# Performance work log

Hardware: AMD Instinct MI355X
Metric: run time of the kernel (lower is better)

The kernel has to match this reference:

```python
import jax, jax.numpy as jnp
import numpy as np

B, C, H, W = 2, 64, 256, 256
CQ = C // 8    # query/key channels
CR = C // 16   # ShareChannelAttention reduction


def _conv1x1(x, w, b):
    # x: [B,C,H,W], w: [O,C], b: [O]  (1x1 conv == per-pixel linear)
    return jnp.einsum('bchw,oc->bohw', x, w) + b[None, :, None, None]


def _criss_cross(q, k, v):
    # q,k: [B,CQ,H,W], v: [B,C,H,W]; row+column attention with -inf on the
    # H-diagonal, softmax over concatenated H+W energies.
    Hh = q.shape[2]
    eH = jnp.einsum('bchw,bcgw->bhwg', q, k)                 # column (over h') energies
    eH = jnp.where(jnp.eye(Hh, dtype=bool)[:, None, :], -jnp.inf, eH)
    eW = jnp.einsum('bchw,bchv->bhwv', q, k)                 # row (over w') energies
    att = jax.nn.softmax(jnp.concatenate([eH, eW], axis=-1), axis=-1)  # [B,H,W,H+W]
    aH, aW = att[..., :Hh], att[..., Hh:]
    outH = jnp.einsum('bhwg,bcgw->bchw', aH, v)
    outW = jnp.einsum('bhwv,bchv->bchw', aW, v)
    return outH + outW


def _shareca(xa, xb, w1, b1, w2, b2):
    s = xa + xb
    def mlp(p):
        return _conv1x1(jax.nn.relu(_conv1x1(p, w1, b1)), w2, b2)
    gate = jax.nn.sigmoid(mlp(s.mean(axis=(2, 3), keepdims=True)) +
                          mlp(s.max(axis=(2, 3), keepdims=True)))
    return gate * s  # gate*xa + gate*xb


def _bn_relu(x, scale, bias):
    # BatchNorm2d in training mode (batch statistics, biased variance), eps=1e-5
    m = x.mean(axis=(0, 2, 3), keepdims=True)
    v = x.var(axis=(0, 2, 3), keepdims=True)
    xn = (x - m) * jax.lax.rsqrt(v + 1e-5)
    return jax.nn.relu(xn * scale[None, :, None, None] + bias[None, :, None, None])


def setup_inputs() -> dict:
    key = jax.random.key(0)
    ks = jax.random.split(key, 32)
    def n(k, shape, s=0.05):
        return jax.random.normal(k, shape, dtype=jnp.float32) * s
    inp = {
        'x1': n(ks[0], (B, C, H, W), 1.0),
        'x2': n(ks[1], (B, C, H, W), 1.0),
        'wq1': n(ks[2], (CQ, C)), 'bq1': n(ks[3], (CQ,)),
        'wq2': n(ks[4], (CQ, C)), 'bq2': n(ks[5], (CQ,)),
        'wk1': n(ks[6], (CQ, C)), 'bk1': n(ks[7], (CQ,)),
        'wk2': n(ks[8], (CQ, C)), 'bk2': n(ks[9], (CQ,)),
        'wv1': n(ks[10], (C, C)), 'bv1': n(ks[11], (C,)),
        'wv2': n(ks[12], (C, C)), 'bv2': n(ks[13], (C,)),
        'gamma1': n(ks[14], (1,), 0.5), 'gamma2': n(ks[15], (1,), 0.5),
        'sc1_w1': n(ks[16], (CR, C)), 'sc1_b1': n(ks[17], (CR,)),
        'sc1_w2': n(ks[18], (C, CR)), 'sc1_b2': n(ks[19], (C,)),
        'sc2_w1': n(ks[20], (CR, C)), 'sc2_b1': n(ks[21], (CR,)),
        'sc2_w2': n(ks[22], (C, CR)), 'sc2_b2': n(ks[23], (C,)),
        'bn1_scale': jnp.ones((C,), jnp.float32), 'bn1_bias': n(ks[24], (C,)),
        'bn2_scale': jnp.ones((C,), jnp.float32), 'bn2_bias': n(ks[25], (C,)),
    }
    return inp


def reference(x1, x2, wq1, bq1, wq2, bq2, wk1, bk1, wk2, bk2,
              wv1, bv1, wv2, bv2, gamma1, gamma2,
              sc1_w1, sc1_b1, sc1_w2, sc1_b2,
              sc2_w1, sc2_b1, sc2_w2, sc2_b2,
              bn1_scale, bn1_bias, bn2_scale, bn2_bias):
    q1 = _conv1x1(x1, wq1, bq1); q2 = _conv1x1(x2, wq2, bq2)
    k1 = _conv1x1(x1, wk1, bk1); k2 = _conv1x1(x2, wk2, bk2)
    v1 = _conv1x1(x1, wv1, bv1); v2 = _conv1x1(x2, wv2, bv2)
    att1 = _criss_cross(q2, k1, v1)  # out_H_1 + out_W_1
    att2 = _criss_cross(q1, k2, v2)  # out_H_2 + out_W_2
    x_1 = _shareca(gamma2 * att2 + x2, x1, sc1_w1, sc1_b1, sc1_w2, sc1_b2)
    x_2 = _shareca(gamma1 * att1 + x1, x2, sc2_w1, sc2_b1, sc2_w2, sc2_b2)
    out1 = _bn_relu(x_1 + x1, bn1_scale, bn1_bias)
    out2 = _bn_relu(x_2 + x2, bn2_scale, bn2_bias)
    # channel exchange: even channels keep the original input
    mask = (jnp.arange(C) % 2 == 0)[None, :, None, None]
    return jnp.where(mask, x1, out1), jnp.where(mask, x2, out2)
```

## Files before the change

kernel.cpp:

```cpp
#include <hip/hip_runtime.h>
#include <hip/hip_bf16.h>
#include <cstdint>
#include <cstddef>

typedef unsigned short bf16t;
typedef __attribute__((ext_vector_type(8))) short bf16x8;
typedef __attribute__((ext_vector_type(4))) float f32x4;

__device__ __forceinline__ unsigned short f2bf(float f) {
    unsigned u = __float_as_uint(f);
    u += 0x7fffu + ((u >> 16) & 1u);
    return (unsigned short)(u >> 16);
}
__device__ __forceinline__ float bf2f(unsigned short h) {
    return __uint_as_float(((unsigned)h) << 16);
}
__device__ __forceinline__ float bflo(unsigned u) { return __uint_as_float(u << 16); }
__device__ __forceinline__ float bfhi(unsigned u) { return __uint_as_float(u & 0xffff0000u); }
__device__ __forceinline__ unsigned pk2(float a, float b) {
    __hip_bfloat162 h = __float22bfloat162_rn(make_float2(a, b));
    return *(unsigned*)&h;
}
__device__ __forceinline__ bf16x8 mk8(unsigned a, unsigned b, unsigned c, unsigned d) {
    union { uint4 u; bf16x8 v; } cv; cv.u = make_uint4(a, b, c, d); return cv.v;
}

__device__ __forceinline__ unsigned fenc(float f) {
    unsigned u = __float_as_uint(f);
    return (u & 0x80000000u) ? ~u : (u | 0x80000000u);
}
__device__ __forceinline__ float fdec(unsigned u) {
    return __uint_as_float((u & 0x80000000u) ? (u ^ 0x80000000u) : ~u);
}

#define HW 65536

struct ConvArgs {
    const float* x[2];
    const float* wq[2]; const float* bq[2];
    const float* wk[2]; const float* bk[2];
    const float* wv[2]; const float* bv[2];
    bf16t* q[2]; bf16t* k[2]; bf16t* v[2];
    unsigned* zeroR;
};

__global__ __launch_bounds__(256) void conv_qkv(ConvArgs A)
{
    __shared__ __align__(16) bf16t Xlds[256 * 68];

    const int t = threadIdx.x;
    const int z = blockIdx.z;
    const int s = z >> 1, b = z & 1;
    if (z == 0 && blockIdx.x == 0) {
#pragma unroll
        for (int i = 0; i < 6; i++) A.zeroR[t + i * 256] = 0u;
    }
    const int lane = t & 63, wv = t >> 6, quad = lane >> 4, l16 = lane & 15;
    const int px0 = blockIdx.x * 256;

    const float* xp = A.x[s] + (size_t)b * 64 * HW + px0 + t;
    {
        unsigned xw[32];
#pragma unroll
        for (int c = 0; c < 32; c++)
            xw[c] = pk2(xp[(size_t)(2 * c) * HW], xp[(size_t)(2 * c + 1) * HW]);
#pragma unroll
        for (int g = 0; g < 16; g++)
            *(uint2*)&Xlds[t * 68 + g * 4] = make_uint2(xw[2 * g], xw[2 * g + 1]);
    }

    bf16x8 bfr[5][2];
    float bo[5];
    bf16t* obase[5];
#pragma unroll
    for (int ot = 0; ot < 5; ot++) {
        const int o = ot * 16 + l16;
        const float* wrow;
        if (o < 8)       { wrow = A.wq[s] + o * 64;        bo[ot] = A.bq[s][o];
                           obase[ot] = A.q[s] + (size_t)(b * 8 + o) * HW; }
        else if (o < 16) { wrow = A.wk[s] + (o - 8) * 64;  bo[ot] = A.bk[s][o - 8];
                           obase[ot] = A.k[s] + (size_t)(b * 8 + o - 8) * HW; }
        else             { wrow = A.wv[s] + (o - 16) * 64; bo[ot] = A.bv[s][o - 16];
                           obase[ot] = A.v[s] + (size_t)(b * 64 + o - 16) * HW; }
#pragma unroll
        for (int ks = 0; ks < 2; ks++) {
            const float* wp = wrow + ks * 32 + quad * 8;
            bfr[ot][ks] = mk8(pk2(wp[0], wp[1]), pk2(wp[2], wp[3]),
                              pk2(wp[4], wp[5]), pk2(wp[6], wp[7]));
        }
    }

    __syncthreads();

    bf16x8 afr[4][2];
#pragma unroll
    for (int i = 0; i < 4; i++)
#pragma unroll
        for (int ks = 0; ks < 2; ks++) {
            const int base = (wv * 64 + i * 16 + l16) * 68 + ks * 32 + quad * 8;
            const uint2 lo = *(const uint2*)&Xlds[base];
            const uint2 hi = *(const uint2*)&Xlds[base + 4];
            afr[i][ks] = mk8(lo.x, lo.y, hi.x, hi.y);
        }

    const f32x4 z4 = {0.f, 0.f, 0.f, 0.f};
    f32x4 acc[4][5];
#pragma unroll
    for (int i = 0; i < 4; i++)
#pragma unroll
        for (int ot = 0; ot < 5; ot++) acc[i][ot] = z4;

#pragma unroll
    for (int ks = 0; ks < 2; ks++)
#pragma unroll
        for (int i = 0; i < 4; i++)
#pragma unroll
            for (int ot = 0; ot < 5; ot++)
                acc[i][ot] = __builtin_amdgcn_mfma_f32_16x16x32_bf16(afr[i][ks], bfr[ot][ks], acc[i][ot], 0, 0, 0);

#pragma unroll
    for (int i = 0; i < 4; i++) {
        const int px = px0 + wv * 64 + i * 16 + quad * 4;
#pragma unroll
        for (int ot = 0; ot < 5; ot++) {
            uint2 u;
            u.x = pk2(acc[i][ot][0] + bo[ot], acc[i][ot][1] + bo[ot]);
            u.y = pk2(acc[i][ot][2] + bo[ot], acc[i][ot][3] + bo[ot]);
            *(uint2*)&obase[ot][px] = u;
        }
    }
}

__global__ __launch_bounds__(256) void transpose16(const bf16t* __restrict__ in, bf16t* __restrict__ out)
{
    __shared__ bf16t tile[64][68];
    const size_t zo = (size_t)blockIdx.z * HW;
    const int i0 = blockIdx.y * 64, j0 = blockIdx.x * 64;
    const int lc = threadIdx.x & 63, rg = threadIdx.x >> 6;
#pragma unroll
    for (int rr = 0; rr < 16; rr++) {
        int row = rg * 16 + rr;
        tile[row][lc] = in[zo + (size_t)(i0 + row) * 256 + j0 + lc];
    }
    __syncthreads();
#pragma unroll
    for (int rr = 0; rr < 16; rr++) {
        int row = rg * 16 + rr;
        out[zo + (size_t)(j0 + row) * 256 + i0 + lc] = tile[lc][row];
    }
}

struct RowccArgs {
    const bf16t* q[4]; const bf16t* k[4]; const bf16t* v[4];
    bf16t* o[4]; float* so[4];
};

__global__ __launch_bounds__(256, 3) void rowcc_mfma(RowccArgs P)
{
    __shared__ __align__(16) char smem[54272];
    bf16t* vs = (bf16t*)smem;
    bf16t* ps = (bf16t*)(smem + 33792);

    const int t = threadIdx.x;
    const int r = blockIdx.x, b = blockIdx.y, z = blockIdx.z;
    const bool mask = (z < 2);
    const int lane = t & 63, wv = t >> 6, quad = lane >> 4, l16 = lane & 15;
    const int wband = wv * 64;

    const bf16t* qp = P.q[z];
    const bf16t* kp = P.k[z];
    const bf16t* vp = P.v[z];

    const size_t vb = (size_t)b * 64 * HW + (size_t)r * 256;
#pragma unroll
    for (int i = 0; i < 8; i++) {
        const int qd = i * 256 + t;
        const int c = qd >> 5, jc = (qd & 31) * 8;
        *(uint4*)&vs[c * 264 + jc] = *(const uint4*)&vp[vb + (size_t)c * HW + jc];
    }

    const bf16x8 zfr = {0, 0, 0, 0, 0, 0, 0, 0};
    bf16x8 qfr[4] = {zfr, zfr, zfr, zfr};
    const size_t rowb = (size_t)b * 8 * HW + (size_t)r * 256;
    if (quad == 0) {
#pragma unroll
        for (int wt = 0; wt < 4; wt++) {
            const int w_g = wband + wt * 16 + l16;
#pragma unroll
            for (int ch = 0; ch < 8; ch++)
                qfr[wt][ch] = (short)qp[rowb + (size_t)ch * HW + w_g];
        }
    }

    const f32x4 z4 = {0.f, 0.f, 0.f, 0.f};
    f32x4 acc[4][4];
#pragma unroll
    for (int i = 0; i < 4; i++)
#pragma unroll
        for (int j = 0; j < 4; j++) acc[i][j] = z4;
    float s_t[4] = {0.f, 0.f, 0.f, 0.f};

    bf16x8 kcur[2] = {zfr, zfr};
    if (quad == 0) {
#pragma unroll
        for (int jtile = 0; jtile < 2; jtile++)
#pragma unroll
            for (int ch = 0; ch < 8; ch++)
                kcur[jtile][ch] = (short)kp[rowb + (size_t)ch * HW + jtile * 16 + l16];
    }

    __syncthreads();

    for (int jt = 0; jt < 8; jt++) {
        const int j0 = jt * 32;
        f32x4 e[4][2];
#pragma unroll
        for (int wt = 0; wt < 4; wt++)
#pragma unroll
            for (int jtile = 0; jtile < 2; jtile++)
                e[wt][jtile] = __builtin_amdgcn_mfma_f32_16x16x32_bf16(kcur[jtile], qfr[wt], z4, 0, 0, 0);

        bf16x8 knext[2] = {zfr, zfr};
        if (jt < 7 && quad == 0) {
            const int jn = (jt + 1) * 32;
#pragma unroll
            for (int jtile = 0; jtile < 2; jtile++)
#pragma unroll
                for (int ch = 0; ch < 8; ch++)
                    knext[jtile][ch] = (short)kp[rowb + (size_t)ch * HW + jn + jtile * 16 + l16];
        }

        if (mask && (jt >> 1) == wv) {
#pragma unroll
            for (int wt = 0; wt < 4; wt++) {
                const int w_g = wband + wt * 16 + l16;
#pragma unroll
                for (int jtile = 0; jtile < 2; jtile++)
#pragma unroll
                    for (int rr = 0; rr < 4; rr++)
                        if (j0 + jtile * 16 + quad * 4 + rr == w_g) e[wt][jtile][rr] = -3.0e38f;
            }
        }

#pragma unroll
        for (int wt = 0; wt < 4; wt++) {
#pragma unroll
            for (int jtile = 0; jtile < 2; jtile++) {
                const float p0 = __expf(e[wt][jtile][0]);
                const float p1 = __expf(e[wt][jtile][1]);
                const float p2 = __expf(e[wt][jtile][2]);
                const float p3 = __expf(e[wt][jtile][3]);
                s_t[wt] += (p0 + p1) + (p2 + p3);
                uint2 u; u.x = pk2(p0, p1); u.y = pk2(p2, p3);
                *(uint2*)&ps[(wband + wt * 16 + l16) * 40 + jtile * 16 + quad * 4] = u;
            }
        }

        bf16x8 afr[4], bfr[4];
#pragma unroll
        for (int wt = 0; wt < 4; wt++)
            afr[wt] = *(const bf16x8*)&ps[(wband + wt * 16 + l16) * 40 + quad * 8];
#pragma unroll
        for (int ct = 0; ct < 4; ct++)
            bfr[ct] = *(const bf16x8*)&vs[(ct * 16 + l16) * 264 + j0 + quad * 8];
#pragma unroll
        for (int wt = 0; wt < 4; wt++)
#pragma unroll
            for (int ct = 0; ct < 4; ct++)
                acc[wt][ct] = __builtin_amdgcn_mfma_f32_16x16x32_bf16(afr[wt], bfr[ct], acc[wt][ct], 0, 0, 0);

        kcur[0] = knext[0]; kcur[1] = knext[1];
    }

#pragma unroll
    for (int wt = 0; wt < 4; wt++) {
        float s = s_t[wt];
        s += __shfl_xor(s, 16, 64);
        s += __shfl_xor(s, 32, 64);
        s_t[wt] = s;
    }
    if (quad == 0) {
#pragma unroll
        for (int wt = 0; wt < 4; wt++) {
            const int w_g = wband + wt * 16 + l16;
            if (mask)
                P.so[z][(size_t)b * HW + w_g * 256 + r] = s_t[wt];
            else
                P.so[z][(size_t)b * HW + r * 256 + w_g] = s_t[wt];
        }
    }

    __syncthreads();
    bf16t* o_lds = (bf16t*)smem;
#pragma unroll
    for (int wt = 0; wt < 4; wt++) {
        const int w0 = wband + wt * 16 + quad * 4;
#pragma unroll
        for (int ct = 0; ct < 4; ct++) {
            const int c = ct * 16 + l16;
            uint2 u;
            u.x = pk2(acc[wt][ct][0], acc[wt][ct][1]);
            u.y = pk2(acc[wt][ct][2], acc[wt][ct][3]);
            *(uint2*)&o_lds[c * 264 + w0] = u;
        }
    }
    __syncthreads();
    bf16t* ob = P.o[z] + (size_t)b * 64 * HW + (size_t)r * 256;
#pragma unroll
    for (int i = 0; i < 8; i++) {
        const int qd = i * 256 + t;
        const int c = qd >> 5, w8 = (qd & 31) * 8;
        *(uint4*)&ob[(size_t)c * HW + w8] = *(const uint4*)&o_lds[c * 264 + w8];
    }
}

__global__ __launch_bounds__(256) void combine_reduce(
    const bf16t* __restrict__ oH1, const bf16t* __restrict__ oW1,
    const bf16t* __restrict__ oH2, const bf16t* __restrict__ oW2,
    const float* __restrict__ sH1, const float* __restrict__ sW1,
    const float* __restrict__ sH2, const float* __restrict__ sW2,
    const float* __restrict__ x1, const float* __restrict__ x2,
    const float* __restrict__ gamma1, const float* __restrict__ gamma2,
    bf16t* __restrict__ s1, bf16t* __restrict__ s2,
    float* __restrict__ accum, unsigned* __restrict__ accmax)
{
    const int t = threadIdx.x, chunk = blockIdx.x, c = blockIdx.y, b = blockIdx.z;
    const float g1v = gamma1[0], g2v = gamma2[0];
    const size_t cb = ((size_t)(b * 64 + c)) * HW;
    const size_t pb = (size_t)b * HW;

    float pS1 = 0, pSS1 = 0, pSX1 = 0, pX1 = 0, pXX1 = 0, pM1 = -3e38f;
    float pS2 = 0, pSS2 = 0, pSX2 = 0, pX2 = 0, pXX2 = 0, pM2 = -3e38f;

    for (int i = 0; i < 16; i++) {
        const int pidx = chunk * 4096 + i * 256 + t;
        const float inv1 = 1.f / (sH1[pb + pidx] + sW1[pb + pidx]);
        const float inv2 = 1.f / (sH2[pb + pidx] + sW2[pb + pidx]);
        const float a1 = (bf2f(oH1[cb + pidx]) + bf2f(oW1[cb + pidx])) * inv1;
        const float a2 = (bf2f(oH2[cb + pidx]) + bf2f(oW2[cb + pidx])) * inv2;
        const float x1v = x1[cb + pidx], x2v = x2[cb + pidx];
        const float s1v = g2v * a2 + x2v + x1v;
        const float s2v = g1v * a1 + x1v + x2v;
        s1[cb + pidx] = f2bf(s1v);
        s2[cb + pidx] = f2bf(s2v);
        pS1 += s1v; pSS1 += s1v * s1v; pSX1 += s1v * x1v; pX1 += x1v; pXX1 += x1v * x1v; pM1 = fmaxf(pM1, s1v);
        pS2 += s2v; pSS2 += s2v * s2v; pSX2 += s2v * x2v; pX2 += x2v; pXX2 += x2v * x2v; pM2 = fmaxf(pM2, s2v);
    }

    __shared__ float wred[12][4];
    float vals[12] = {pS1, pSS1, pSX1, pX1, pXX1, pM1, pS2, pSS2, pSX2, pX2, pXX2, pM2};
    const int lane = t & 63, wave = t >> 6;
#pragma unroll
    for (int iv = 0; iv < 12; iv++) {
        float v = vals[iv];
        const bool isMax = (iv == 5 || iv == 11);
#pragma unroll
        for (int off = 32; off > 0; off >>= 1) {
            const float o = __shfl_down(v, off, 64);
            v = isMax ? fmaxf(v, o) : (v + o);
        }
        if (lane == 0) wred[iv][wave] = v;
    }
    __syncthreads();
    if (t < 12) {
        const bool isMax = (t == 5 || t == 11);
        float v = wred[t][0];
        for (int i = 1; i < 4; i++) v = isMax ? fmaxf(v, wred[t][i]) : (v + wred[t][i]);
        const int stream = (t >= 6) ? 1 : 0;
        const int kk = t - stream * 6;
        if (kk == 5) atomicMax(&accmax[(stream * 2 + b) * 64 + c], fenc(v));
        else atomicAdd(&accum[((stream * 2 + b) * 64 + c) * 5 + kk], v);
    }
}

__global__ __launch_bounds__(256) void gates_bn(
    const float* __restrict__ accum, const unsigned* __restrict__ accmax,
    const float* __restrict__ sc1_w1, const float* __restrict__ sc1_b1,
    const float* __restrict__ sc1_w2, const float* __restrict__ sc1_b2,
    const float* __restrict__ sc2_w1, const float* __restrict__ sc2_b1,
    const float* __restrict__ sc2_w2, const float* __restrict__ sc2_b2,
    const float* __restrict__ bn1_scale, const float* __restrict__ bn1_bias,
    const float* __restrict__ bn2_scale, const float* __restrict__ bn2_bias,
    float* __restrict__ gates, float* __restrict__ AB)
{
    const int t = threadIdx.x;
    const int stream = t >> 7, b = (t >> 6) & 1, c = t & 63;
    __shared__ float meanS[256], maxS[256], e1S[256], e2S[256];

    const float S = accum[t * 5 + 0], SS = accum[t * 5 + 1], SX = accum[t * 5 + 2];
    const float X = accum[t * 5 + 3], XX = accum[t * 5 + 4];
    meanS[t] = S * (1.f / 65536.f);
    maxS[t] = fdec(accmax[t]);
    __syncthreads();

    const float* w1 = stream ? sc2_w1 : sc1_w1;
    const float* b1 = stream ? sc2_b1 : sc1_b1;
    const float* w2 = stream ? sc2_w2 : sc1_w2;
    const float* b2 = stream ? sc2_b2 : sc1_b2;
    float om = b2[c], ox = b2[c];
    const int base = stream * 128 + b * 64;
#pragma unroll
    for (int r = 0; r < 4; r++) {
        float hm = b1[r], hx = b1[r];
        for (int cc = 0; cc < 64; cc++) {
            hm += w1[r * 64 + cc] * meanS[base + cc];
            hx += w1[r * 64 + cc] * maxS[base + cc];
        }
        hm = fmaxf(hm, 0.f); hx = fmaxf(hx, 0.f);
        om += w2[c * 4 + r] * hm;
        ox += w2[c * 4 + r] * hx;
    }
    const float gate = 1.f / (1.f + __expf(-(om + ox)));
    gates[t] = gate;
    e1S[t] = gate * S + X;
    e2S[t] = gate * gate * SS + 2.f * gate * SX + XX;
    __syncthreads();
    if (b == 0) {
        const float sumY = e1S[t] + e1S[t + 64];
        const float sumY2 = e2S[t] + e2S[t + 64];
        const float meanY = sumY * (1.f / 131072.f);
        const float varY = sumY2 * (1.f / 131072.f) - meanY * meanY;
        const float sc = stream ? bn2_scale[c] : bn1_scale[c];
        const float bi = stream ? bn2_bias[c] : bn1_bias[c];
        const float A = sc * rsqrtf(varY + 1e-5f);
        AB[stream * 128 + c] = A;
        AB[stream * 128 + 64 + c] = bi - meanY * A;
    }
}

__global__ __launch_bounds__(256) void finalize(
    const bf16t* __restrict__ s1, const bf16t* __restrict__ s2,
    const float* __restrict__ x1, const float* __restrict__ x2,
    const float* __restrict__ gates, const float* __restrict__ AB,
    float* __restrict__ out)
{
    const size_t tid = (size_t)blockIdx.x * 256 + threadIdx.x;
    const size_t idx = tid * 4;
    const int b = (int)(idx >> 22);
    const int c = (int)((idx >> 16) & 63);
    const bool odd = (c & 1) != 0;
    const float g1 = gates[b * 64 + c], g2 = gates[128 + b * 64 + c];
    const float A1 = AB[c], B1 = AB[64 + c], A2 = AB[128 + c], B2 = AB[192 + c];

    const uint2 su1 = *(const uint2*)(s1 + idx);
    const uint2 su2 = *(const uint2*)(s2 + idx);
    const float4 x1v = *(const float4*)(x1 + idx);
    const float4 x2v = *(const float4*)(x2 + idx);
    float s1f[4] = {bflo(su1.x), bfhi(su1.x), bflo(su1.y), bfhi(su1.y)};
    float s2f[4] = {bflo(su2.x), bfhi(su2.x), bflo(su2.y), bfhi(su2.y)};
    float xa[4] = {x1v.x, x1v.y, x1v.z, x1v.w};
    float xb[4] = {x2v.x, x2v.y, x2v.z, x2v.w};
    float o1[4], o2[4];
#pragma unroll
    for (int j = 0; j < 4; j++) {
        const float y1 = g1 * s1f[j] + xa[j];
        const float y2 = g2 * s2f[j] + xb[j];
        o1[j] = odd ? fmaxf(A1 * y1 + B1, 0.f) : xa[j];
        o2[j] = odd ? fmaxf(A2 * y2 + B2, 0.f) : xb[j];
    }
    *(float4*)(out + idx) = make_float4(o1[0], o1[1], o1[2], o1[3]);
    *(float4*)(out + 8388608 + idx) = make_float4(o2[0], o2[1], o2[2], o2[3]);
}

extern "C" void kernel_launch(void* const* d_in, const int* in_sizes, int n_in,
                              void* d_out, int out_size, void* d_ws, size_t ws_size,
                              hipStream_t stream) {
    (void)in_sizes; (void)n_in; (void)out_size; (void)ws_size;
    const float* x1 = (const float*)d_in[0];
    const float* x2 = (const float*)d_in[1];
    const float* wq1 = (const float*)d_in[2];  const float* bq1 = (const float*)d_in[3];
    const float* wq2 = (const float*)d_in[4];  const float* bq2 = (const float*)d_in[5];
    const float* wk1 = (const float*)d_in[6];  const float* bk1 = (const float*)d_in[7];
    const float* wk2 = (const float*)d_in[8];  const float* bk2 = (const float*)d_in[9];
    const float* wv1 = (const float*)d_in[10]; const float* bv1 = (const float*)d_in[11];
    const float* wv2 = (const float*)d_in[12]; const float* bv2 = (const float*)d_in[13];
    const float* gamma1 = (const float*)d_in[14];
    const float* gamma2 = (const float*)d_in[15];
    const float* sc1_w1 = (const float*)d_in[16]; const float* sc1_b1 = (const float*)d_in[17];
    const float* sc1_w2 = (const float*)d_in[18]; const float* sc1_b2 = (const float*)d_in[19];
    const float* sc2_w1 = (const float*)d_in[20]; const float* sc2_b1 = (const float*)d_in[21];
    const float* sc2_w2 = (const float*)d_in[22]; const float* sc2_b2 = (const float*)d_in[23];
    const float* bn1_scale = (const float*)d_in[24]; const float* bn1_bias = (const float*)d_in[25];
    const float* bn2_scale = (const float*)d_in[26]; const float* bn2_bias = (const float*)d_in[27];

    char* p = (char*)d_ws;
    const size_t SZ_QK = 2097152;
    const size_t SZ_V = 16777216;
    const size_t SZ_ST = 524288;

    bf16t* q1 = (bf16t*)(p + 0 * SZ_QK);
    bf16t* k1 = (bf16t*)(p + 1 * SZ_QK);
    bf16t* q2 = (bf16t*)(p + 2 * SZ_QK);
    bf16t* k2 = (bf16t*)(p + 3 * SZ_QK);
    bf16t* v1 = (bf16t*)(p + 4 * SZ_QK);
    bf16t* v2 = (bf16t*)(p + 4 * SZ_QK + SZ_V);
    size_t off = 4 * SZ_QK + 2 * SZ_V;
    bf16t* q1T = (bf16t*)(p + off + 0 * SZ_QK);
    bf16t* k1T = (bf16t*)(p + off + 1 * SZ_QK);
    bf16t* q2T = (bf16t*)(p + off + 2 * SZ_QK);
    bf16t* k2T = (bf16t*)(p + off + 3 * SZ_QK);
    bf16t* v1T = (bf16t*)(p + off + 4 * SZ_QK);
    bf16t* v2T = (bf16t*)(p + off + 4 * SZ_QK + SZ_V);
    off += 4 * SZ_QK + 2 * SZ_V;
    bf16t* oH1T = (bf16t*)(p + off); off += SZ_V;
    bf16t* oH2T = (bf16t*)(p + off); off += SZ_V;
    bf16t* oW1 = (bf16t*)(p + off); off += SZ_V;
    bf16t* oW2 = (bf16t*)(p + off); off += SZ_V;
    float* sH1 = (float*)(p + off); off += SZ_ST;
    float* sH2 = (float*)(p + off); off += SZ_ST;
    float* sW1 = (float*)(p + off); off += SZ_ST;
    float* sW2 = (float*)(p + off); off += SZ_ST;
    float* accum = (float*)(p + off);
    unsigned* accmax = (unsigned*)(p + off + 5120);
    float* gates = (float*)(p + off + 6144);
    float* AB = (float*)(p + off + 7168);

    bf16t* oH1 = v1T;
    bf16t* oH2 = v2T;
    bf16t* s1 = oH1T;
    bf16t* s2 = oH2T;

    ConvArgs CA;
    CA.x[0] = x1; CA.x[1] = x2;
    CA.wq[0] = wq1; CA.wq[1] = wq2; CA.bq[0] = bq1; CA.bq[1] = bq2;
    CA.wk[0] = wk1; CA.wk[1] = wk2; CA.bk[0] = bk1; CA.bk[1] = bk2;
    CA.wv[0] = wv1; CA.wv[1] = wv2; CA.bv[0] = bv1; CA.bv[1] = bv2;
    CA.q[0] = q1; CA.q[1] = q2; CA.k[0] = k1; CA.k[1] = k2;
    CA.v[0] = v1; CA.v[1] = v2;
    CA.zeroR = (unsigned*)accum;
    conv_qkv<<<dim3(256, 1, 4), 256, 0, stream>>>(CA);

    transpose16<<<dim3(4, 4, 320), 256, 0, stream>>>(q1, q1T);

    RowccArgs RA;
    RA.q[0] = q2T; RA.k[0] = k1T; RA.v[0] = v1T; RA.o[0] = oH1T; RA.so[0] = sH1;
    RA.q[1] = q1T; RA.k[1] = k2T; RA.v[1] = v2T; RA.o[1] = oH2T; RA.so[1] = sH2;
    RA.q[2] = q2;  RA.k[2] = k1;  RA.v[2] = v1;  RA.o[2] = oW1;  RA.so[2] = sW1;
    RA.q[3] = q1;  RA.k[3] = k2;  RA.v[3] = v2;  RA.o[3] = oW2;  RA.so[3] = sW2;
    rowcc_mfma<<<dim3(256, 2, 4), 256, 0, stream>>>(RA);

    transpose16<<<dim3(4, 4, 256), 256, 0, stream>>>(oH1T, oH1);

    combine_reduce<<<dim3(16, 64, 2), 256, 0, stream>>>(
        oH1, oW1, oH2, oW2, sH1, sW1, sH2, sW2, x1, x2, gamma1, gamma2,
        s1, s2, accum, accmax);

    gates_bn<<<1, 256, 0, stream>>>(accum, accmax,
                                    sc1_w1, sc1_b1, sc1_w2, sc1_b2,
                                    sc2_w1, sc2_b1, sc2_w2, sc2_b2,
                                    bn1_scale, bn1_bias, bn2_scale, bn2_bias,
                                    gates, AB);

    finalize<<<8192, 256, 0, stream>>>(s1, s2, x1, x2, gates, AB, (float*)d_out);
}
```

Before: 323.4 us.

## Fold log2e into Q, stage K/Q in LDS, pipeline scores, fuse gates and drop transpose

The attention kernel now stages the K and Q rows in LDS and computes the next tile's scores while the PV MFMAs run, using exp2 with log2e folded into the query conv weights. The transpose of the column-attention output is removed; combine_reduce reads the transposed layout directly. The separate gates/BN kernel is merged into combine_reduce through a last-block-done atomic counter. The changes cut launches, extra memory passes and exp cost, but combine_reduce now reads with a strided access pattern and rowcc occupancy drops from 3 to 2 blocks.

```diff
diff --git a/kernel.cpp b/kernel.cpp
--- a/kernel.cpp
+++ b/kernel.cpp
@@ -24,7 +24,6 @@
 __device__ __forceinline__ bf16x8 mk8(unsigned a, unsigned b, unsigned c, unsigned d) {
     union { uint4 u; bf16x8 v; } cv; cv.u = make_uint4(a, b, c, d); return cv.v;
 }
-
 __device__ __forceinline__ unsigned fenc(float f) {
     unsigned u = __float_as_uint(f);
     return (u & 0x80000000u) ? ~u : (u | 0x80000000u);
@@ -34,6 +33,7 @@
 }
 
 #define HW 65536
+#define LOG2E 1.4426950408889634f
 
 struct ConvArgs {
     const float* x[2];
@@ -53,7 +53,7 @@
     const int s = z >> 1, b = z & 1;
     if (z == 0 && blockIdx.x == 0) {
 #pragma unroll
-        for (int i = 0; i < 6; i++) A.zeroR[t + i * 256] = 0u;
+        for (int i = 0; i < 7; i++) A.zeroR[t + i * 256] = 0u;
     }
     const int lane = t & 63, wv = t >> 6, quad = lane >> 4, l16 = lane & 15;
     const int px0 = blockIdx.x * 256;
@@ -76,7 +76,8 @@
     for (int ot = 0; ot < 5; ot++) {
         const int o = ot * 16 + l16;
         const float* wrow;
-        if (o < 8)       { wrow = A.wq[s] + o * 64;        bo[ot] = A.bq[s][o];
+        float wsc = 1.f;
+        if (o < 8)       { wrow = A.wq[s] + o * 64;        bo[ot] = A.bq[s][o] * LOG2E; wsc = LOG2E;
                            obase[ot] = A.q[s] + (size_t)(b * 8 + o) * HW; }
         else if (o < 16) { wrow = A.wk[s] + (o - 8) * 64;  bo[ot] = A.bk[s][o - 8];
                            obase[ot] = A.k[s] + (size_t)(b * 8 + o - 8) * HW; }
@@ -85,8 +86,8 @@
 #pragma unroll
         for (int ks = 0; ks < 2; ks++) {
             const float* wp = wrow + ks * 32 + quad * 8;
-            bfr[ot][ks] = mk8(pk2(wp[0], wp[1]), pk2(wp[2], wp[3]),
-                              pk2(wp[4], wp[5]), pk2(wp[6], wp[7]));
+            bfr[ot][ks] = mk8(pk2(wp[0] * wsc, wp[1] * wsc), pk2(wp[2] * wsc, wp[3] * wsc),
+                              pk2(wp[4] * wsc, wp[5] * wsc), pk2(wp[6] * wsc, wp[7] * wsc));
         }
     }
 
@@ -155,11 +156,13 @@
     bf16t* o[4]; float* so[4];
 };
 
-__global__ __launch_bounds__(256, 3) void rowcc_mfma(RowccArgs P)
+__global__ __launch_bounds__(256, 2) void rowcc_mfma(RowccArgs P)
 {
-    __shared__ __align__(16) char smem[54272];
+    __shared__ __align__(16) char smem[62464];
     bf16t* vs = (bf16t*)smem;
     bf16t* ps = (bf16t*)(smem + 33792);
+    bf16t* ks = (bf16t*)(smem + 54272);
+    bf16t* qs = (bf16t*)(smem + 58368);
 
     const int t = threadIdx.x;
     const int r = blockIdx.x, b = blockIdx.y, z = blockIdx.z;
@@ -171,6 +174,21 @@
     const bf16t* kp = P.k[z];
     const bf16t* vp = P.v[z];
 
+    const size_t rowb = (size_t)b * 8 * HW + (size_t)r * 256 + t;
+    {
+        const bf16t* kq = kp + rowb;
+        unsigned w0 = (unsigned)kq[0] | ((unsigned)kq[(size_t)HW] << 16);
+        unsigned w1 = (unsigned)kq[2 * (size_t)HW] | ((unsigned)kq[3 * (size_t)HW] << 16);
+        unsigned w2 = (unsigned)kq[4 * (size_t)HW] | ((unsigned)kq[5 * (size_t)HW] << 16);
+        unsigned w3 = (unsigned)kq[6 * (size_t)HW] | ((unsigned)kq[7 * (size_t)HW] << 16);
+        *(uint4*)&ks[t * 8] = make_uint4(w0, w1, w2, w3);
+        const bf16t* qq = qp + rowb;
+        w0 = (unsigned)qq[0] | ((unsigned)qq[(size_t)HW] << 16);
+        w1 = (unsigned)qq[2 * (size_t)HW] | ((unsigned)qq[3 * (size_t)HW] << 16);
+        w2 = (unsigned)qq[4 * (size_t)HW] | ((unsigned)qq[5 * (size_t)HW] << 16);
+        w3 = (unsigned)qq[6 * (size_t)HW] | ((unsigned)qq[7 * (size_t)HW] << 16);
+        *(uint4*)&qs[t * 8] = make_uint4(w0, w1, w2, w3);
+    }
     const size_t vb = (size_t)b * 64 * HW + (size_t)r * 256;
 #pragma unroll
     for (int i = 0; i < 8; i++) {
@@ -179,20 +197,17 @@
         *(uint4*)&vs[c * 264 + jc] = *(const uint4*)&vp[vb + (size_t)c * HW + jc];
     }
 
+    __syncthreads();
+
     const bf16x8 zfr = {0, 0, 0, 0, 0, 0, 0, 0};
-    bf16x8 qfr[4] = {zfr, zfr, zfr, zfr};
-    const size_t rowb = (size_t)b * 8 * HW + (size_t)r * 256;
-    if (quad == 0) {
-#pragma unroll
-        for (int wt = 0; wt < 4; wt++) {
-            const int w_g = wband + wt * 16 + l16;
-#pragma unroll
-            for (int ch = 0; ch < 8; ch++)
-                qfr[wt][ch] = (short)qp[rowb + (size_t)ch * HW + w_g];
-        }
-    }
-
     const f32x4 z4 = {0.f, 0.f, 0.f, 0.f};
+    bf16x8 qfr[4];
+#pragma unroll
+    for (int wt = 0; wt < 4; wt++) {
+        bf16x8 v8 = *(const bf16x8*)&qs[(wband + wt * 16 + l16) * 8];
+        qfr[wt] = (quad == 0) ? v8 : zfr;
+    }
+
     f32x4 acc[4][4];
 #pragma unroll
     for (int i = 0; i < 4; i++)
@@ -200,37 +215,18 @@
         for (int j = 0; j < 4; j++) acc[i][j] = z4;
     float s_t[4] = {0.f, 0.f, 0.f, 0.f};
 
-    bf16x8 kcur[2] = {zfr, zfr};
-    if (quad == 0) {
-#pragma unroll
-        for (int jtile = 0; jtile < 2; jtile++)
-#pragma unroll
-            for (int ch = 0; ch < 8; ch++)
-                kcur[jtile][ch] = (short)kp[rowb + (size_t)ch * HW + jtile * 16 + l16];
-    }
-
-    __syncthreads();
-
-    for (int jt = 0; jt < 8; jt++) {
-        const int j0 = jt * 32;
-        f32x4 e[4][2];
-#pragma unroll
-        for (int wt = 0; wt < 4; wt++)
-#pragma unroll
-            for (int jtile = 0; jtile < 2; jtile++)
-                e[wt][jtile] = __builtin_amdgcn_mfma_f32_16x16x32_bf16(kcur[jtile], qfr[wt], z4, 0, 0, 0);
-
-        bf16x8 knext[2] = {zfr, zfr};
-        if (jt < 7 && quad == 0) {
-            const int jn = (jt + 1) * 32;
-#pragma unroll
-            for (int jtile = 0; jtile < 2; jtile++)
-#pragma unroll
-                for (int ch = 0; ch < 8; ch++)
-                    knext[jtile][ch] = (short)kp[rowb + (size_t)ch * HW + jn + jtile * 16 + l16];
-        }
-
+    auto scores = [&](int jt, f32x4 (&e)[4][2]) {
+        bf16x8 kfr0 = *(const bf16x8*)&ks[(jt * 32 + l16) * 8];
+        bf16x8 kfr1 = *(const bf16x8*)&ks[(jt * 32 + 16 + l16) * 8];
+#pragma unroll
+        for (int wt = 0; wt < 4; wt++) {
+            e[wt][0] = __builtin_amdgcn_mfma_f32_16x16x32_bf16(kfr0, qfr[wt], z4, 0, 0, 0);
+            e[wt][1] = __builtin_amdgcn_mfma_f32_16x16x32_bf16(kfr1, qfr[wt], z4, 0, 0, 0);
+        }
+    };
+    auto expstore = [&](int jt, f32x4 (&e)[4][2]) {
         if (mask && (jt >> 1) == wv) {
+            const int j0m = jt * 32;
 #pragma unroll
             for (int wt = 0; wt < 4; wt++) {
                 const int w_g = wband + wt * 16 + l16;
@@ -238,24 +234,32 @@
                 for (int jtile = 0; jtile < 2; jtile++)
 #pragma unroll
                     for (int rr = 0; rr < 4; rr++)
-                        if (j0 + jtile * 16 + quad * 4 + rr == w_g) e[wt][jtile][rr] = -3.0e38f;
+                        if (j0m + jtile * 16 + quad * 4 + rr == w_g) e[wt][jtile][rr] = -3.0e38f;
             }
         }
-
 #pragma unroll
         for (int wt = 0; wt < 4; wt++) {
 #pragma unroll
             for (int jtile = 0; jtile < 2; jtile++) {
-                const float p0 = __expf(e[wt][jtile][0]);
-                const float p1 = __expf(e[wt][jtile][1]);
-                const float p2 = __expf(e[wt][jtile][2]);
-                const float p3 = __expf(e[wt][jtile][3]);
+                const float p0 = __builtin_amdgcn_exp2f(e[wt][jtile][0]);
+                const float p1 = __builtin_amdgcn_exp2f(e[wt][jtile][1]);
+                const float p2 = __builtin_amdgcn_exp2f(e[wt][jtile][2]);
+                const float p3 = __builtin_amdgcn_exp2f(e[wt][jtile][3]);
                 s_t[wt] += (p0 + p1) + (p2 + p3);
                 uint2 u; u.x = pk2(p0, p1); u.y = pk2(p2, p3);
                 *(uint2*)&ps[(wband + wt * 16 + l16) * 40 + jtile * 16 + quad * 4] = u;
             }
         }
-
+    };
+
+    {
+        f32x4 e0[4][2];
+        scores(0, e0);
+        expstore(0, e0);
+    }
+
+    for (int jt = 0; jt < 8; jt++) {
+        const int j0 = jt * 32;
         bf16x8 afr[4], bfr[4];
 #pragma unroll
         for (int wt = 0; wt < 4; wt++)
@@ -263,13 +267,17 @@
 #pragma unroll
         for (int ct = 0; ct < 4; ct++)
             bfr[ct] = *(const bf16x8*)&vs[(ct * 16 + l16) * 264 + j0 + quad * 8];
+
+        f32x4 en[4][2];
+        if (jt < 7) scores(jt + 1, en);
+
 #pragma unroll
         for (int wt = 0; wt < 4; wt++)
 #pragma unroll
             for (int ct = 0; ct < 4; ct++)
                 acc[wt][ct] = __builtin_amdgcn_mfma_f32_16x16x32_bf16(afr[wt], bfr[ct], acc[wt][ct], 0, 0, 0);
 
-        kcur[0] = knext[0]; kcur[1] = knext[1];
+        if (jt < 7) expstore(jt + 1, en);
     }
 
 #pragma unroll
@@ -283,10 +291,7 @@
 #pragma unroll
         for (int wt = 0; wt < 4; wt++) {
             const int w_g = wband + wt * 16 + l16;
-            if (mask)
-                P.so[z][(size_t)b * HW + w_g * 256 + r] = s_t[wt];
-            else
-                P.so[z][(size_t)b * HW + r * 256 + w_g] = s_t[wt];
+            P.so[z][(size_t)b * HW + r * 256 + w_g] = s_t[wt];
         }
     }
 
@@ -315,14 +320,21 @@
 }
 
 __global__ __launch_bounds__(256) void combine_reduce(
-    const bf16t* __restrict__ oH1, const bf16t* __restrict__ oW1,
-    const bf16t* __restrict__ oH2, const bf16t* __restrict__ oW2,
-    const float* __restrict__ sH1, const float* __restrict__ sW1,
-    const float* __restrict__ sH2, const float* __restrict__ sW2,
+    const bf16t* __restrict__ oH1T, const bf16t* __restrict__ oW1,
+    const bf16t* __restrict__ oH2T, const bf16t* __restrict__ oW2,
+    const float* __restrict__ sH1T, const float* __restrict__ sW1,
+    const float* __restrict__ sH2T, const float* __restrict__ sW2,
     const float* __restrict__ x1, const float* __restrict__ x2,
     const float* __restrict__ gamma1, const float* __restrict__ gamma2,
     bf16t* __restrict__ s1, bf16t* __restrict__ s2,
-    float* __restrict__ accum, unsigned* __restrict__ accmax)
+    float* __restrict__ accum, unsigned* __restrict__ accmax, unsigned* __restrict__ done,
+    const float* __restrict__ sc1_w1, const float* __restrict__ sc1_b1,
+    const float* __restrict__ sc1_w2, const float* __restrict__ sc1_b2,
+    const float* __restrict__ sc2_w1, const float* __restrict__ sc2_b1,
+    const float* __restrict__ sc2_w2, const float* __restrict__ sc2_b2,
+    const float* __restrict__ bn1_scale, const float* __restrict__ bn1_bias,
+    const float* __restrict__ bn2_scale, const float* __restrict__ bn2_bias,
+    float* __restrict__ gates, float* __restrict__ AB)
 {
     const int t = threadIdx.x, chunk = blockIdx.x, c = blockIdx.y, b = blockIdx.z;
     const float g1v = gamma1[0], g2v = gamma2[0];
@@ -333,11 +345,14 @@
     float pS2 = 0, pSS2 = 0, pSX2 = 0, pX2 = 0, pXX2 = 0, pM2 = -3e38f;
 
     for (int i = 0; i < 16; i++) {
-        const int pidx = chunk * 4096 + i * 256 + t;
-        const float inv1 = 1.f / (sH1[pb + pidx] + sW1[pb + pidx]);
-        const float inv2 = 1.f / (sH2[pb + pidx] + sW2[pb + pidx]);
-        const float a1 = (bf2f(oH1[cb + pidx]) + bf2f(oW1[cb + pidx])) * inv1;
-        const float a2 = (bf2f(oH2[cb + pidx]) + bf2f(oW2[cb + pidx])) * inv2;
+        const int h = chunk * 16 + i;
+        const int pidx = h * 256 + t;
+        const size_t tI = pb + (size_t)t * 256 + h;
+        const size_t trI = cb + (size_t)t * 256 + h;
+        const float inv1 = 1.f / (sH1T[tI] + sW1[pb + pidx]);
+        const float inv2 = 1.f / (sH2T[tI] + sW2[pb + pidx]);
+        const float a1 = (bf2f(oH1T[trI]) + bf2f(oW1[cb + pidx])) * inv1;
+        const float a2 = (bf2f(oH2T[trI]) + bf2f(oW2[cb + pidx])) * inv2;
         const float x1v = x1[cb + pidx], x2v = x2[cb + pidx];
         const float s1v = g2v * a2 + x2v + x1v;
         const float s2v = g1v * a1 + x1v + x2v;
@@ -371,60 +386,60 @@
         if (kk == 5) atomicMax(&accmax[(stream * 2 + b) * 64 + c], fenc(v));
         else atomicAdd(&accum[((stream * 2 + b) * 64 + c) * 5 + kk], v);
     }
-}
-
-__global__ __launch_bounds__(256) void gates_bn(
-    const float* __restrict__ accum, const unsigned* __restrict__ accmax,
-    const float* __restrict__ sc1_w1, const float* __restrict__ sc1_b1,
-    const float* __restrict__ sc1_w2, const float* __restrict__ sc1_b2,
-    const float* __restrict__ sc2_w1, const float* __restrict__ sc2_b1,
-    const float* __restrict__ sc2_w2, const float* __restrict__ sc2_b2,
-    const float* __restrict__ bn1_scale, const float* __restrict__ bn1_bias,
-    const float* __restrict__ bn2_scale, const float* __restrict__ bn2_bias,
-    float* __restrict__ gates, float* __restrict__ AB)
-{
-    const int t = threadIdx.x;
-    const int stream = t >> 7, b = (t >> 6) & 1, c = t & 63;
+
+    __threadfence();
+    __shared__ int lastFlag;
+    __syncthreads();
+    if (t == 0) lastFlag = (atomicAdd(done, 1u) == 2047u) ? 1 : 0;
+    __syncthreads();
+    if (!lastFlag) return;
+    __threadfence();
+
     __shared__ float meanS[256], maxS[256], e1S[256], e2S[256];
-
-    const float S = accum[t * 5 + 0], SS = accum[t * 5 + 1], SX = accum[t * 5 + 2];
-    const float X = accum[t * 5 + 3], XX = accum[t * 5 + 4];
-    meanS[t] = S * (1.f / 65536.f);
-    maxS[t] = fdec(accmax[t]);
-    __syncthreads();
-
-    const float* w1 = stream ? sc2_w1 : sc1_w1;
-    const float* b1 = stream ? sc2_b1 : sc1_b1;
-    const float* w2 = stream ? sc2_w2 : sc1_w2;
-    const float* b2 = stream ? sc2_b2 : sc1_b2;
-    float om = b2[c], ox = b2[c];
-    const int base = stream * 128 + b * 64;
-#pragma unroll
-    for (int r = 0; r < 4; r++) {
-        float hm = b1[r], hx = b1[r];
-        for (int cc = 0; cc < 64; cc++) {
-            hm += w1[r * 64 + cc] * meanS[base + cc];
-            hx += w1[r * 64 + cc] * maxS[base + cc];
-        }
-        hm = fmaxf(hm, 0.f); hx = fmaxf(hx, 0.f);
-        om += w2[c * 4 + r] * hm;
-        ox += w2[c * 4 + r] * hx;
-    }
-    const float gate = 1.f / (1.f + __expf(-(om + ox)));
-    gates[t] = gate;
-    e1S[t] = gate * S + X;
-    e2S[t] = gate * gate * SS + 2.f * gate * SX + XX;
-    __syncthreads();
-    if (b == 0) {
-        const float sumY = e1S[t] + e1S[t + 64];
-        const float sumY2 = e2S[t] + e2S[t + 64];
-        const float meanY = sumY * (1.f / 131072.f);
-        const float varY = sumY2 * (1.f / 131072.f) - meanY * meanY;
-        const float sc = stream ? bn2_scale[c] : bn1_scale[c];
-        const float bi = stream ? bn2_bias[c] : bn1_bias[c];
-        const float A = sc * rsqrtf(varY + 1e-5f);
-        AB[stream * 128 + c] = A;
-        AB[stream * 128 + 64 + c] = bi - meanY * A;
+    {
+        const int stream = t >> 7, bb = (t >> 6) & 1, cc = t & 63;
+        const float S  = atomicAdd(&accum[t * 5 + 0], 0.f);
+        const float SS = atomicAdd(&accum[t * 5 + 1], 0.f);
+        const float SX = atomicAdd(&accum[t * 5 + 2], 0.f);
+        const float X  = atomicAdd(&accum[t * 5 + 3], 0.f);
+        const float XX = atomicAdd(&accum[t * 5 + 4], 0.f);
+        meanS[t] = S * (1.f / 65536.f);
+        maxS[t] = fdec(atomicAdd(&accmax[t], 0u));
+        __syncthreads();
+
+        const float* w1 = stream ? sc2_w1 : sc1_w1;
+        const float* b1 = stream ? sc2_b1 : sc1_b1;
+        const float* w2 = stream ? sc2_w2 : sc1_w2;
+        const float* b2 = stream ? sc2_b2 : sc1_b2;
+        float om = b2[cc], ox = b2[cc];
+        const int base = stream * 128 + bb * 64;
+#pragma unroll
+        for (int rr = 0; rr < 4; rr++) {
+            float hm = b1[rr], hx = b1[rr];
+            for (int c2 = 0; c2 < 64; c2++) {
+                hm += w1[rr * 64 + c2] * meanS[base + c2];
+                hx += w1[rr * 64 + c2] * maxS[base + c2];
+            }
+            hm = fmaxf(hm, 0.f); hx = fmaxf(hx, 0.f);
+            om += w2[cc * 4 + rr] * hm;
+            ox += w2[cc * 4 + rr] * hx;
+        }
+        const float gate = 1.f / (1.f + __expf(-(om + ox)));
+        gates[t] = gate;
+        e1S[t] = gate * S + X;
+        e2S[t] = gate * gate * SS + 2.f * gate * SX + XX;
+        __syncthreads();
+        if (bb == 0) {
+            const float sumY = e1S[t] + e1S[t + 64];
+            const float sumY2 = e2S[t] + e2S[t + 64];
+            const float meanY = sumY * (1.f / 131072.f);
+            const float varY = sumY2 * (1.f / 131072.f) - meanY * meanY;
+            const float sc = stream ? bn2_scale[cc] : bn1_scale[cc];
+            const float bi = stream ? bn2_bias[cc] : bn1_bias[cc];
+            const float Aa = sc * rsqrtf(varY + 1e-5f);
+            AB[stream * 128 + cc] = Aa;
+            AB[stream * 128 + 64 + cc] = bi - meanY * Aa;
+        }
     }
 }
 
@@ -512,13 +527,12 @@
     float* sW2 = (float*)(p + off); off += SZ_ST;
     float* accum = (float*)(p + off);
     unsigned* accmax = (unsigned*)(p + off + 5120);
-    float* gates = (float*)(p + off + 6144);
-    float* AB = (float*)(p + off + 7168);
-
-    bf16t* oH1 = v1T;
-    bf16t* oH2 = v2T;
-    bf16t* s1 = oH1T;
-    bf16t* s2 = oH2T;
+    unsigned* done = (unsigned*)(p + off + 6144);
+    float* gates = (float*)(p + off + 7168);
+    float* AB = (float*)(p + off + 8192);
+
+    bf16t* s1 = v1T;
+    bf16t* s2 = v2T;
 
     ConvArgs CA;
     CA.x[0] = x1; CA.x[1] = x2;
@@ -539,17 +553,13 @@
     RA.q[3] = q1;  RA.k[3] = k2;  RA.v[3] = v2;  RA.o[3] = oW2;  RA.so[3] = sW2;
     rowcc_mfma<<<dim3(256, 2, 4), 256, 0, stream>>>(RA);
 
-    transpose16<<<dim3(4, 4, 256), 256, 0, stream>>>(oH1T, oH1);
-
     combine_reduce<<<dim3(16, 64, 2), 256, 0, stream>>>(
-        oH1, oW1, oH2, oW2, sH1, sW1, sH2, sW2, x1, x2, gamma1, gamma2,
-        s1, s2, accum, accmax);
-
-    gates_bn<<<1, 256, 0, stream>>>(accum, accmax,
-                                    sc1_w1, sc1_b1, sc1_w2, sc1_b2,
-                                    sc2_w1, sc2_b1, sc2_w2, sc2_b2,
-                                    bn1_scale, bn1_bias, bn2_scale, bn2_bias,
-                                    gates, AB);
+        oH1T, oW1, oH2T, oW2, sH1, sW1, sH2, sW2, x1, x2, gamma1, gamma2,
+        s1, s2, accum, accmax, done,
+        sc1_w1, sc1_b1, sc1_w2, sc1_b2,
+        sc2_w1, sc2_b1, sc2_w2, sc2_b2,
+        bn1_scale, bn1_bias, bn2_scale, bn2_bias,
+        gates, AB);
 
     finalize<<<8192, 256, 0, stream>>>(s1, s2, x1, x2, gates, AB, (float*)d_out);
 }
```

Result: slower. 752.3 us (+132.6%).
